# Kernel optimization log

Measured on AMD Instinct MI355X. Metric: run time of the kernel, lower is better.

Reference implementation:

```python
import jax, jax.numpy as jnp
import numpy as np

NU, NI = 40000, 60000
N = NU + NI            # total nodes
DF, DL, DI = 1024, 128, 64
E = 1600000            # number of edges
SLOPE = 0.01           # torch leaky_relu default negative slope
EPS = 1e-12            # torch F.normalize eps


def _leaky(v):
    return jnp.where(v > 0, v, SLOPE * v)


def setup_inputs() -> dict:
    key = jax.random.key(0)
    ks = jax.random.split(key, 17)
    s = 0.02  # xavier-ish scale for weights
    return {
        "features": jax.random.normal(ks[0], (NI, DF), jnp.float32),
        "id_embedding": jax.random.normal(ks[1], (N, DI), jnp.float32),
        "preference": jax.random.normal(ks[2], (NU, DL), jnp.float32) * s,
        "mlp_w": jax.random.normal(ks[3], (DL, DF), jnp.float32) * s,
        "mlp_b": jnp.zeros((DL,), jnp.float32),
        "conv1_w": jax.random.normal(ks[4], (DL, DL), jnp.float32) * s,
        "lin1_w": jax.random.normal(ks[5], (DI, DL), jnp.float32) * s,
        "lin1_b": jnp.zeros((DI,), jnp.float32),
        "g1_w": jax.random.normal(ks[6], (DI, DL), jnp.float32) * s,
        "g1_b": jnp.zeros((DI,), jnp.float32),
        "conv2_w": jax.random.normal(ks[7], (DI, DI), jnp.float32) * s,
        "lin2_w": jax.random.normal(ks[8], (DI, DI), jnp.float32) * s,
        "lin2_b": jnp.zeros((DI,), jnp.float32),
        "g2_w": jax.random.normal(ks[9], (DI, DI), jnp.float32) * s,
        "g2_b": jnp.zeros((DI,), jnp.float32),
        "edge_index": jax.random.randint(ks[10], (2, E), 0, N, jnp.int32),
    }


def reference(features, id_embedding, preference, mlp_w, mlp_b,
              conv1_w, lin1_w, lin1_b, g1_w, g1_b,
              conv2_w, lin2_w, lin2_b, g2_w, g2_b, edge_index):
    src, dst = edge_index[0], edge_index[1]

    # MLP on item features, concat with user preference -> [N, DL]
    temp = features @ mlp_w.T + mlp_b
    x = jnp.concatenate([preference, temp], axis=0)
    # row-wise L2 normalize (F.normalize dim=1)
    x = x / jnp.clip(jnp.linalg.norm(x, axis=1, keepdims=True), EPS)

    # ----- layer 1 -----
    xw = x @ conv1_w                                      # [N, DL]
    h = _leaky(jax.ops.segment_sum(xw[src], dst, num_segments=N))
    x_hat = _leaky(x @ lin1_w.T + lin1_b) + id_embedding  # [N, DI]
    x = _leaky(h @ g1_w.T + g1_b + x_hat)                 # [N, DI]

    # ----- layer 2 -----
    xw = x @ conv2_w                                      # [N, DI]
    h = _leaky(jax.ops.segment_sum(xw[src], dst, num_segments=N))
    x_hat = _leaky(x @ lin2_w.T + lin2_b) + id_embedding
    x = _leaky(h @ g2_w.T + g2_b + x_hat)
    return x
```

## Files before the change

kernel.cpp:

```cpp
#include <hip/hip_runtime.h>
#include <hip/hip_bf16.h>

typedef __hip_bfloat16 bf16;
typedef __bf16 bf16x8 __attribute__((ext_vector_type(8)));
typedef float f32x4 __attribute__((ext_vector_type(4)));

#define NU 40000
#define NI 60000
#define NN 100000
#define DF 1024
#define DL 128
#define DI 64
#define NE 1600000
#define CAP 64

__device__ __forceinline__ float leaky(float v) { return v > 0.0f ? v : 0.01f * v; }

__device__ __forceinline__ unsigned short f2b(float f) {
    unsigned u = __builtin_bit_cast(unsigned, f);
    unsigned r = (u + 0x7FFFu + ((u >> 16) & 1u)) >> 16;
    return (unsigned short)r;
}
__device__ __forceinline__ bf16 tobf(float f) {
    unsigned short r = f2b(f);
    return __builtin_bit_cast(bf16, r);
}
__device__ __forceinline__ unsigned pk2(float x, float y) {
    return (unsigned)f2b(x) | ((unsigned)f2b(y) << 16);
}
template<typename T>
__device__ __forceinline__ void stage8(bf16* dst, const T* src) {
    if constexpr (sizeof(T) == 2) {
        *(uint4*)dst = *(const uint4*)src;
    } else {
        float4 a = *(const float4*)src;
        float4 b = *(const float4*)(src + 4);
        uint2 lo, hi;
        lo.x = pk2(a.x, a.y); lo.y = pk2(a.z, a.w);
        hi.x = pk2(b.x, b.y); hi.y = pk2(b.z, b.w);
        *(uint2*)dst = lo;
        *(uint2*)(dst + 4) = hi;
    }
}
__device__ __forceinline__ void zero8(bf16* dst) {
    uint4 z = {0u, 0u, 0u, 0u};
    *(uint4*)dst = z;
}

__global__ void csr_fill(const int* __restrict__ ei, int* __restrict__ cnt,
                         int* __restrict__ bucket) {
    int e = blockIdx.x * 256 + threadIdx.x;
    if (e >= NE) return;
    int s = ei[e];
    int d = ei[NE + e];
    int p = atomicAdd(&cnt[d], 1);
    if (p < CAP) bucket[d * CAP + p] = s;
}

template<int K, int M>
__global__ void transpose_kernel(const float* __restrict__ W, bf16* __restrict__ Wt) {
    int idx = blockIdx.x * 256 + threadIdx.x;
    if (idx < K * M) {
        int k = idx / M, m = idx % M;
        Wt[m * K + k] = tobf(W[k * M + m]);
    }
}

__global__ __launch_bounds__(256) void gemm1_kernel(const float* __restrict__ A,
                                                    const float* __restrict__ W,
                                                    const float* __restrict__ bias,
                                                    bf16* __restrict__ out) {
    __shared__ __align__(16) bf16 As[128 * 64];
    __shared__ __align__(16) bf16 Bs[128 * 64];
    int t = threadIdx.x;
    int wave = t >> 6, lane = t & 63;
    int q = lane >> 4, l16 = lane & 15;
    int row0 = blockIdx.x * 128;
    f32x4 acc[2][8] = {};
    for (int k0 = 0; k0 < DF; k0 += 64) {
        #pragma unroll
        for (int i = 0; i < 4; i++) {
            int slot = t + i * 256;
            int r = slot >> 3;
            int kc = (slot & 7) * 8;
            int gr = row0 + r;
            if (gr < NI) stage8(As + r * 64 + kc, A + (size_t)gr * DF + k0 + kc);
            else         zero8(As + r * 64 + kc);
            stage8(Bs + r * 64 + kc, W + (size_t)r * DF + k0 + kc);
        }
        __syncthreads();
        #pragma unroll
        for (int kk = 0; kk < 64; kk += 32) {
            bf16x8 a0 = *(const bf16x8*)(As + (wave * 32 + l16) * 64 + kk + q * 8);
            bf16x8 a1 = *(const bf16x8*)(As + (wave * 32 + 16 + l16) * 64 + kk + q * 8);
            #pragma unroll
            for (int nt = 0; nt < 8; nt++) {
                bf16x8 b = *(const bf16x8*)(Bs + (nt * 16 + l16) * 64 + kk + q * 8);
                acc[0][nt] = __builtin_amdgcn_mfma_f32_16x16x32_bf16(a0, b, acc[0][nt], 0, 0, 0);
                acc[1][nt] = __builtin_amdgcn_mfma_f32_16x16x32_bf16(a1, b, acc[1][nt], 0, 0, 0);
            }
        }
        __syncthreads();
    }
    #pragma unroll
    for (int mt = 0; mt < 2; mt++) {
        #pragma unroll
        for (int nt = 0; nt < 8; nt++) {
            int col = nt * 16 + l16;
            float bv = bias[col];
            #pragma unroll
            for (int r = 0; r < 4; r++) {
                int row = row0 + wave * 32 + mt * 16 + q * 4 + r;
                if (row < NI) out[(size_t)row * DL + col] = tobf(acc[mt][nt][r] + bv);
            }
        }
    }
}

__global__ __launch_bounds__(256) void norm_kernel(const float* __restrict__ pref,
                                                   const bf16* __restrict__ temp,
                                                   bf16* __restrict__ x0) {
    __shared__ float wsum[4];
    int t = threadIdx.x;
    int g = t >> 7;
    int c = t & 127;
    int row = blockIdx.x * 2 + g;
    float v = (row < NU) ? pref[(size_t)row * DL + c]
                         : (float)temp[(size_t)(row - NU) * DL + c];
    float ss = v * v;
    #pragma unroll
    for (int off = 32; off > 0; off >>= 1) ss += __shfl_down(ss, off);
    int wave = t >> 6;
    if ((t & 63) == 0) wsum[wave] = ss;
    __syncthreads();
    float tot = wsum[g * 2] + wsum[g * 2 + 1];
    float inv = 1.0f / fmaxf(sqrtf(tot), 1e-12f);
    x0[(size_t)row * DL + c] = tobf(v * inv);
}

template<typename WT, int K, int M, int EPI, typename OutT>
__global__ __launch_bounds__(256) void sgemm_kernel(const bf16* __restrict__ A,
                                                    const WT* __restrict__ Wt,
                                                    const float* __restrict__ bias,
                                                    const float* __restrict__ extra,
                                                    OutT* __restrict__ out,
                                                    int nrows) {
    __shared__ __align__(16) bf16 As[128 * K];
    __shared__ __align__(16) bf16 Ws[M * K];
    int t = threadIdx.x;
    int wave = t >> 6, lane = t & 63;
    int q = lane >> 4, l16 = lane & 15;
    int row0 = blockIdx.x * 128;
    constexpr int WSLOT = M * K / 8;
    for (int slot = t; slot < WSLOT; slot += 256)
        stage8(Ws + slot * 8, Wt + (size_t)slot * 8);
    constexpr int SLOTS = 128 * K / 8;
    for (int slot = t; slot < SLOTS; slot += 256) {
        int r = slot / (K / 8);
        int kc = (slot % (K / 8)) * 8;
        int gr = row0 + r;
        if (gr < nrows) *(uint4*)(As + r * K + kc) = *(const uint4*)(A + (size_t)gr * K + kc);
        else            zero8(As + r * K + kc);
    }
    __syncthreads();
    constexpr int NT = M / 16;
    f32x4 acc[2][NT] = {};
    #pragma unroll
    for (int kk = 0; kk < K; kk += 32) {
        bf16x8 a0 = *(const bf16x8*)(As + (wave * 32 + l16) * K + kk + q * 8);
        bf16x8 a1 = *(const bf16x8*)(As + (wave * 32 + 16 + l16) * K + kk + q * 8);
        #pragma unroll
        for (int nt = 0; nt < NT; nt++) {
            bf16x8 b = *(const bf16x8*)(Ws + (nt * 16 + l16) * K + kk + q * 8);
            acc[0][nt] = __builtin_amdgcn_mfma_f32_16x16x32_bf16(a0, b, acc[0][nt], 0, 0, 0);
            acc[1][nt] = __builtin_amdgcn_mfma_f32_16x16x32_bf16(a1, b, acc[1][nt], 0, 0, 0);
        }
    }
    #pragma unroll
    for (int mt = 0; mt < 2; mt++) {
        #pragma unroll
        for (int nt = 0; nt < NT; nt++) {
            int col = nt * 16 + l16;
            float bv = (EPI != 0) ? bias[col] : 0.0f;
            #pragma unroll
            for (int r = 0; r < 4; r++) {
                int row = row0 + wave * 32 + mt * 16 + q * 4 + r;
                if (row < nrows) {
                    float z = acc[mt][nt][r];
                    if (EPI == 1) {
                        z = leaky(z + bv) + extra[(size_t)row * M + col];
                    } else if (EPI == 2) {
                        z = leaky(z + bv + extra[(size_t)row * M + col]);
                    }
                    if constexpr (sizeof(OutT) == 2) out[(size_t)row * M + col] = tobf(z);
                    else                             out[(size_t)row * M + col] = z;
                }
            }
        }
    }
}

template<int D>
__global__ __launch_bounds__(256) void gather_kernel(const bf16* __restrict__ xw,
                                                     const int* __restrict__ cnt,
                                                     const int* __restrict__ bucket,
                                                     bf16* __restrict__ h) {
    constexpr int GP = 256 / D;
    __shared__ int srcs[GP][CAP];
    int g = threadIdx.x / D;
    int c = threadIdx.x % D;
    int node = blockIdx.x * GP + g;
    int deg = min(cnt[node], CAP);
    for (int i = c; i < deg; i += D) srcs[g][i] = bucket[node * CAP + i];
    __syncthreads();
    float sum = 0.0f;
    for (int i = 0; i < deg; i++) {
        int s = srcs[g][i];
        sum += (float)xw[(size_t)s * D + c];
    }
    h[(size_t)node * D + c] = tobf(leaky(sum));
}

extern "C" void kernel_launch(void* const* d_in, const int* in_sizes, int n_in,
                              void* d_out, int out_size, void* d_ws, size_t ws_size,
                              hipStream_t stream) {
    const void* p[16];
    for (int i = 0; i < 16 && i < n_in; i++) p[i] = d_in[i];
    if (n_in == 16) {
        int n8192 = 0, n4096 = 0, n64 = 0;
        const int idx64[4] = {7, 9, 12, 14};
        const int idx4096[3] = {10, 11, 13};
        for (int i = 0; i < 16; i++) {
            switch (in_sizes[i]) {
                case 61440000: p[0] = d_in[i]; break;
                case 6400000:  p[1] = d_in[i]; break;
                case 5120000:  p[2] = d_in[i]; break;
                case 131072:   p[3] = d_in[i]; break;
                case 128:      p[4] = d_in[i]; break;
                case 16384:    p[5] = d_in[i]; break;
                case 8192:     p[n8192++ ? 8 : 6] = d_in[i]; break;
                case 64:       if (n64 < 4) p[idx64[n64++]] = d_in[i]; break;
                case 4096:     if (n4096 < 3) p[idx4096[n4096++]] = d_in[i]; break;
                case 3200000:  p[15] = d_in[i]; break;
                default: break;
            }
        }
    }
    const float* features = (const float*)p[0];
    const float* id_emb   = (const float*)p[1];
    const float* pref     = (const float*)p[2];
    const float* mlp_w    = (const float*)p[3];
    const float* mlp_b    = (const float*)p[4];
    const float* conv1_w  = (const float*)p[5];
    const float* lin1_w   = (const float*)p[6];
    const float* lin1_b   = (const float*)p[7];
    const float* g1_w     = (const float*)p[8];
    const float* g1_b     = (const float*)p[9];
    const float* conv2_w  = (const float*)p[10];
    const float* lin2_w   = (const float*)p[11];
    const float* lin2_b   = (const float*)p[12];
    const float* g2_w     = (const float*)p[13];
    const float* g2_b     = (const float*)p[14];
    const int*   ei       = (const int*)p[15];

    char* wsp = (char*)d_ws;
    size_t off = 0;
    auto alloc = [&](size_t bytes) {
        void* ptr = wsp + off;
        off += (bytes + 255) & ~(size_t)255;
        return ptr;
    };
    void* regA = alloc((size_t)NN * DL * 2);
    void* regB = alloc((size_t)NN * DL * 2);
    void* regC = alloc((size_t)NN * DL * 2);
    int*  cnt    = (int*) alloc((size_t)NN * 4);
    int*  bucket = (int*) alloc((size_t)NN * CAP * 4);
    bf16* c1t    = (bf16*)alloc((size_t)DL * DL * 2);
    bf16* c2t    = (bf16*)alloc((size_t)DI * DI * 2);

    bf16*  temp = (bf16*)regA;
    bf16*  h1   = (bf16*)regA;
    bf16*  h2   = (bf16*)regA;
    bf16*  x0   = (bf16*)regB;
    bf16*  xw2  = (bf16*)regB;
    bf16*  xw1  = (bf16*)regC;
    float* xhat = (float*)regC;
    bf16*  x1   = (bf16*)d_out;
    float* out  = (float*)d_out;

    hipMemsetAsync(cnt, 0, (size_t)NN * 4, stream);
    csr_fill<<<NE / 256, 256, 0, stream>>>(ei, cnt, bucket);

    transpose_kernel<DL, DL><<<(DL * DL + 255) / 256, 256, 0, stream>>>(conv1_w, c1t);
    transpose_kernel<DI, DI><<<(DI * DI + 255) / 256, 256, 0, stream>>>(conv2_w, c2t);

    gemm1_kernel<<<(NI + 127) / 128, 256, 0, stream>>>(features, mlp_w, mlp_b, temp);
    norm_kernel<<<NN / 2, 256, 0, stream>>>(pref, temp, x0);

    const int SG = (NN + 127) / 128;
    sgemm_kernel<bf16, DL, DL, 0, bf16><<<SG, 256, 0, stream>>>(x0, c1t, nullptr, nullptr, xw1, NN);
    gather_kernel<DL><<<NN / 2, 256, 0, stream>>>(xw1, cnt, bucket, h1);
    sgemm_kernel<float, DL, DI, 1, float><<<SG, 256, 0, stream>>>(x0, lin1_w, lin1_b, id_emb, xhat, NN);
    sgemm_kernel<float, DL, DI, 2, bf16><<<SG, 256, 0, stream>>>(h1, g1_w, g1_b, xhat, x1, NN);
    sgemm_kernel<float, DI, DI, 1, float><<<SG, 256, 0, stream>>>(x1, lin2_w, lin2_b, id_emb, xhat, NN);
    sgemm_kernel<bf16, DI, DI, 0, bf16><<<SG, 256, 0, stream>>>(x1, c2t, nullptr, nullptr, xw2, NN);
    gather_kernel<DI><<<NN / 4, 256, 0, stream>>>(xw2, cnt, bucket, h2);
    sgemm_kernel<float, DI, DI, 2, float><<<SG, 256, 0, stream>>>(h2, g2_w, g2_b, xhat, out, NN);
}
```

Baseline: 880.1 us.

## Double-buffer feature GEMM with swizzled LDS, pre-convert weights, vectorize gathers

```diff
diff --git a/kernel.cpp b/kernel.cpp
--- a/kernel.cpp
+++ b/kernel.cpp
@@ -28,6 +28,9 @@
 __device__ __forceinline__ unsigned pk2(float x, float y) {
     return (unsigned)f2b(x) | ((unsigned)f2b(y) << 16);
 }
+__device__ __forceinline__ float b2f_lo(unsigned u) { return __builtin_bit_cast(float, u << 16); }
+__device__ __forceinline__ float b2f_hi(unsigned u) { return __builtin_bit_cast(float, u & 0xffff0000u); }
+
 template<typename T>
 __device__ __forceinline__ void stage8(bf16* dst, const T* src) {
     if constexpr (sizeof(T) == 2) {
@@ -66,52 +69,112 @@
     }
 }
 
+__global__ void convert_kernel(const float* __restrict__ W, bf16* __restrict__ out) {
+    int i = blockIdx.x * 256 + threadIdx.x;
+    float4 v = *(const float4*)(W + (size_t)i * 4);
+    uint2 p;
+    p.x = pk2(v.x, v.y);
+    p.y = pk2(v.z, v.w);
+    *(uint2*)(out + (size_t)i * 4) = p;
+}
+
 __global__ __launch_bounds__(256) void gemm1_kernel(const float* __restrict__ A,
-                                                    const float* __restrict__ W,
+                                                    const bf16* __restrict__ Wb,
                                                     const float* __restrict__ bias,
                                                     bf16* __restrict__ out) {
-    __shared__ __align__(16) bf16 As[128 * 64];
-    __shared__ __align__(16) bf16 Bs[128 * 64];
+    __shared__ __align__(16) bf16 As[2][64 * 64];
+    __shared__ __align__(16) bf16 Bs[2][128 * 64];
     int t = threadIdx.x;
-    int wave = t >> 6, lane = t & 63;
-    int q = lane >> 4, l16 = lane & 15;
-    int row0 = blockIdx.x * 128;
-    f32x4 acc[2][8] = {};
-    for (int k0 = 0; k0 < DF; k0 += 64) {
-        #pragma unroll
-        for (int i = 0; i < 4; i++) {
-            int slot = t + i * 256;
-            int r = slot >> 3;
-            int kc = (slot & 7) * 8;
-            int gr = row0 + r;
-            if (gr < NI) stage8(As + r * 64 + kc, A + (size_t)gr * DF + k0 + kc);
-            else         zero8(As + r * 64 + kc);
-            stage8(Bs + r * 64 + kc, W + (size_t)r * DF + k0 + kc);
-        }
-        __syncthreads();
+    int wave = t >> 6, lane = t & 63, q = lane >> 4, l16 = lane & 15;
+    int wm = wave >> 1, wn = wave & 1;
+    int row0 = blockIdx.x * 64;
+
+    const float* ap[2];
+    const bf16* bp[4];
+    int aoff[2], boff[4];
+    bool aval[2];
+    #pragma unroll
+    for (int i = 0; i < 2; i++) {
+        int slot = t + i * 256;
+        int r = slot >> 3, kc = (slot & 7) * 8;
+        ap[i] = A + (size_t)(row0 + r) * DF + kc;
+        aval[i] = (row0 + r) < NI;
+        aoff[i] = r * 64 + (((kc >> 3) ^ (r & 7)) << 3);
+    }
+    #pragma unroll
+    for (int i = 0; i < 4; i++) {
+        int slot = t + i * 256;
+        int r = slot >> 3, kc = (slot & 7) * 8;
+        bp[i] = Wb + (size_t)r * DF + kc;
+        boff[i] = r * 64 + (((kc >> 3) ^ (r & 7)) << 3);
+    }
+
+    float4 av[2][2];
+    uint4 bv[4];
+    auto issue = [&](int k0) {
+        #pragma unroll
+        for (int i = 0; i < 2; i++) {
+            if (aval[i]) {
+                av[i][0] = *(const float4*)(ap[i] + k0);
+                av[i][1] = *(const float4*)(ap[i] + k0 + 4);
+            } else {
+                av[i][0] = float4{0.f, 0.f, 0.f, 0.f};
+                av[i][1] = float4{0.f, 0.f, 0.f, 0.f};
+            }
+        }
+        #pragma unroll
+        for (int i = 0; i < 4; i++) bv[i] = *(const uint4*)(bp[i] + k0);
+    };
+    auto commit = [&](int buf) {
+        #pragma unroll
+        for (int i = 0; i < 2; i++) {
+            uint4 pkd;
+            pkd.x = pk2(av[i][0].x, av[i][0].y);
+            pkd.y = pk2(av[i][0].z, av[i][0].w);
+            pkd.z = pk2(av[i][1].x, av[i][1].y);
+            pkd.w = pk2(av[i][1].z, av[i][1].w);
+            *(uint4*)(&As[buf][aoff[i]]) = pkd;
+        }
+        #pragma unroll
+        for (int i = 0; i < 4; i++) *(uint4*)(&Bs[buf][boff[i]]) = bv[i];
+    };
+
+    f32x4 acc[2][4] = {};
+    issue(0);
+    commit(0);
+    __syncthreads();
+    for (int k0i = 0; k0i < 16; k0i++) {
+        int buf = k0i & 1;
+        if (k0i < 15) issue((k0i + 1) * 64);
         #pragma unroll
         for (int kk = 0; kk < 64; kk += 32) {
-            bf16x8 a0 = *(const bf16x8*)(As + (wave * 32 + l16) * 64 + kk + q * 8);
-            bf16x8 a1 = *(const bf16x8*)(As + (wave * 32 + 16 + l16) * 64 + kk + q * 8);
+            int ch = (kk >> 3) + q;
+            int ra = wm * 32 + l16;
+            bf16x8 a0 = *(const bf16x8*)&As[buf][ra * 64 + ((ch ^ (ra & 7)) << 3)];
+            bf16x8 a1 = *(const bf16x8*)&As[buf][(ra + 16) * 64 + ((ch ^ (ra & 7)) << 3)];
             #pragma unroll
-            for (int nt = 0; nt < 8; nt++) {
-                bf16x8 b = *(const bf16x8*)(Bs + (nt * 16 + l16) * 64 + kk + q * 8);
+            for (int nt = 0; nt < 4; nt++) {
+                int rb = wn * 64 + nt * 16 + l16;
+                bf16x8 b = *(const bf16x8*)&Bs[buf][rb * 64 + ((ch ^ (rb & 7)) << 3)];
                 acc[0][nt] = __builtin_amdgcn_mfma_f32_16x16x32_bf16(a0, b, acc[0][nt], 0, 0, 0);
                 acc[1][nt] = __builtin_amdgcn_mfma_f32_16x16x32_bf16(a1, b, acc[1][nt], 0, 0, 0);
             }
         }
-        __syncthreads();
+        if (k0i < 15) {
+            commit(buf ^ 1);
+            __syncthreads();
+        }
     }
     #pragma unroll
     for (int mt = 0; mt < 2; mt++) {
         #pragma unroll
-        for (int nt = 0; nt < 8; nt++) {
-            int col = nt * 16 + l16;
-            float bv = bias[col];
+        for (int nt = 0; nt < 4; nt++) {
+            int col = wn * 64 + nt * 16 + l16;
+            float bvv = bias[col];
             #pragma unroll
             for (int r = 0; r < 4; r++) {
-                int row = row0 + wave * 32 + mt * 16 + q * 4 + r;
-                if (row < NI) out[(size_t)row * DL + col] = tobf(acc[mt][nt][r] + bv);
+                int row = row0 + wm * 32 + mt * 16 + q * 4 + r;
+                if (row < NI) out[(size_t)row * DL + col] = tobf(acc[mt][nt][r] + bvv);
             }
         }
     }
@@ -205,20 +268,27 @@
                                                      const int* __restrict__ cnt,
                                                      const int* __restrict__ bucket,
                                                      bf16* __restrict__ h) {
-    constexpr int GP = 256 / D;
+    constexpr int TPN = D / 4;
+    constexpr int GP = 256 / TPN;
     __shared__ int srcs[GP][CAP];
-    int g = threadIdx.x / D;
-    int c = threadIdx.x % D;
+    int g = threadIdx.x / TPN;
+    int c = threadIdx.x % TPN;
     int node = blockIdx.x * GP + g;
     int deg = min(cnt[node], CAP);
-    for (int i = c; i < deg; i += D) srcs[g][i] = bucket[node * CAP + i];
+    for (int i = c; i < deg; i += TPN) srcs[g][i] = bucket[node * CAP + i];
     __syncthreads();
-    float sum = 0.0f;
+    const uint2* x2 = (const uint2*)xw;
+    float s0 = 0.0f, s1 = 0.0f, s2 = 0.0f, s3 = 0.0f;
     for (int i = 0; i < deg; i++) {
         int s = srcs[g][i];
-        sum += (float)xw[(size_t)s * D + c];
-    }
-    h[(size_t)node * D + c] = tobf(leaky(sum));
+        uint2 v = x2[(size_t)s * (D / 4) + c];
+        s0 += b2f_lo(v.x); s1 += b2f_hi(v.x);
+        s2 += b2f_lo(v.y); s3 += b2f_hi(v.y);
+    }
+    uint2 o;
+    o.x = pk2(leaky(s0), leaky(s1));
+    o.y = pk2(leaky(s2), leaky(s3));
+    *(uint2*)(h + (size_t)node * D + c * 4) = o;
 }
 
 extern "C" void kernel_launch(void* const* d_in, const int* in_sizes, int n_in,
@@ -283,6 +353,7 @@
     bf16*  h2   = (bf16*)regA;
     bf16*  x0   = (bf16*)regB;
     bf16*  xw2  = (bf16*)regB;
+    bf16*  mwb  = (bf16*)regC;
     bf16*  xw1  = (bf16*)regC;
     float* xhat = (float*)regC;
     bf16*  x1   = (bf16*)d_out;
@@ -293,17 +364,18 @@
 
     transpose_kernel<DL, DL><<<(DL * DL + 255) / 256, 256, 0, stream>>>(conv1_w, c1t);
     transpose_kernel<DI, DI><<<(DI * DI + 255) / 256, 256, 0, stream>>>(conv2_w, c2t);
-
-    gemm1_kernel<<<(NI + 127) / 128, 256, 0, stream>>>(features, mlp_w, mlp_b, temp);
+    convert_kernel<<<(DL * DF) / 1024, 256, 0, stream>>>(mlp_w, mwb);
+
+    gemm1_kernel<<<(NI + 63) / 64, 256, 0, stream>>>(features, mwb, mlp_b, temp);
     norm_kernel<<<NN / 2, 256, 0, stream>>>(pref, temp, x0);
 
     const int SG = (NN + 127) / 128;
     sgemm_kernel<bf16, DL, DL, 0, bf16><<<SG, 256, 0, stream>>>(x0, c1t, nullptr, nullptr, xw1, NN);
-    gather_kernel<DL><<<NN / 2, 256, 0, stream>>>(xw1, cnt, bucket, h1);
+    gather_kernel<DL><<<NN / 8, 256, 0, stream>>>(xw1, cnt, bucket, h1);
     sgemm_kernel<float, DL, DI, 1, float><<<SG, 256, 0, stream>>>(x0, lin1_w, lin1_b, id_emb, xhat, NN);
     sgemm_kernel<float, DL, DI, 2, bf16><<<SG, 256, 0, stream>>>(h1, g1_w, g1_b, xhat, x1, NN);
     sgemm_kernel<float, DI, DI, 1, float><<<SG, 256, 0, stream>>>(x1, lin2_w, lin2_b, id_emb, xhat, NN);
     sgemm_kernel<bf16, DI, DI, 0, bf16><<<SG, 256, 0, stream>>>(x1, c2t, nullptr, nullptr, xw2, NN);
-    gather_kernel<DI><<<NN / 4, 256, 0, stream>>>(xw2, cnt, bucket, h2);
+    gather_kernel<DI><<<NN / 16, 256, 0, stream>>>(xw2, cnt, bucket, h2);
     sgemm_kernel<float, DI, DI, 2, float><<<SG, 256, 0, stream>>>(h2, g2_w, g2_b, xhat, out, NN);
 }
```

New measurement: 806.9 us. -8.3%, faster.
